# Optimization experiments

Measured on AMD Instinct MI355X. Metric: run time of the kernel, lower is better.

Reference implementation:

```python
import jax, jax.numpy as jnp
import numpy as np
from jax import lax

B, H, W, K, L = 4096, 128, 128, 2, 4
GAMMA = 1e-4  # kernel_gamma
THRESHOLD = 0.0


def setup_inputs() -> dict:
    key = jax.random.key(0)
    ks = jax.random.split(key, 10)
    data = jax.random.normal(ks[0], (B, 1, H, W), jnp.float32)
    conv_w = jax.random.normal(ks[1], (1, 1, K, K), jnp.float32) * 0.5  # OIHW
    conv_b = jax.random.normal(ks[2], (1,), jnp.float32) * 0.1
    # fraud layers: Linear(2,2) weight/bias + affine scale/shift per layer.
    # layers after the first are clamped to [-5,5] at construction time.
    fraud_W = jax.random.normal(ks[3], (L, 2, 2), jnp.float32) * 0.5
    fraud_b = jax.random.normal(ks[4], (L, 2), jnp.float32) * 0.5
    fraud_W = fraud_W.at[1:].set(jnp.clip(fraud_W[1:], -5.0, 5.0))
    fraud_b = fraud_b.at[1:].set(jnp.clip(fraud_b[1:], -5.0, 5.0))
    scale = jax.random.normal(ks[5], (L, 2), jnp.float32)
    shift = jax.random.normal(ks[6], (L, 2), jnp.float32) * 0.1
    final_W = jax.random.normal(ks[7], (1, 2), jnp.float32) * 0.5
    final_b = jax.random.normal(ks[8], (1,), jnp.float32) * 0.1
    return {"data": data, "conv_w": conv_w, "conv_b": conv_b,
            "fraud_W": fraud_W, "fraud_b": fraud_b, "scale": scale,
            "shift": shift, "final_W": final_W, "final_b": final_b}


def reference(data, conv_w, conv_b, fraud_W, fraud_b, scale, shift, final_W, final_b):
    # conv2d(1->1, k=2, valid) + bias, then sigmoid(x - threshold)
    conv = lax.conv_general_dilated(
        data, conv_w, window_strides=(1, 1), padding="VALID",
        dimension_numbers=("NCHW", "OIHW", "NCHW"))
    conv = conv + conv_b[None, :, None, None]
    conv_out = jax.nn.sigmoid(conv - THRESHOLD)
    conv_mean = conv_out.mean(axis=(2, 3))          # [B, 1]
    x = conv_mean.reshape(-1, 2)                    # [B//2, 2] (shape fix)

    def step(carry, p):
        Wl, bl, sl, shl = p
        return jnp.tanh(carry @ Wl.T + bl) * sl + shl, None

    x, _ = lax.scan(step, x, (fraud_W, fraud_b, scale, shift))
    fraud_out = x @ final_W.T + final_b             # [B//2, 1]
    # RBF kernel against zeros over the flattened output -> scalar
    flat = fraud_out.reshape(1, -1)
    k_val = jnp.exp(-GAMMA * jnp.sum(flat * flat, axis=-1, keepdims=True))
    return k_val.squeeze()
```

## Files before the change

kernel.cpp:

```cpp
#include <hip/hip_runtime.h>

#define IMG_H 128
#define IMG_W 128
#define OUT_H 127
#define OUT_W 127

__global__ __launch_bounds__(256) void conv_sig_sum_kernel(
    const float* __restrict__ data,
    const float* __restrict__ conv_w,
    const float* __restrict__ conv_b,
    float* __restrict__ img_sum)
{
    const int b    = blockIdx.x;
    const float* img = data + (size_t)b * (IMG_H * IMG_W);
    const int tid  = threadIdx.x;
    const int wid  = tid >> 6;
    const int lane = tid & 63;

    const float w00 = conv_w[0], w01 = conv_w[1];
    const float w10 = conv_w[2], w11 = conv_w[3];
    const float bias = conv_b[0];

    const int r0 = wid * 32;
    const int r1 = min(r0 + 32, OUT_H);

    float acc = 0.f;

    const float* rt = img + r0 * IMG_W;
    float t0  = rt[lane];
    float t0n = rt[lane + 1];
    float t1  = rt[64 + lane];
    float t1n = (lane < 63) ? rt[65 + lane] : 0.f;

    for (int r = r0; r < r1; ++r) {
        const float* rb = img + (r + 1) * IMG_W;
        float b0  = rb[lane];
        float b0n = rb[lane + 1];
        float b1  = rb[64 + lane];
        float b1n = (lane < 63) ? rb[65 + lane] : 0.f;

        {
            float v = w00 * t0 + w01 * t0n + w10 * b0 + w11 * b0n + bias;
            float e = __expf(-v);
            acc += __builtin_amdgcn_rcpf(1.0f + e);
        }
        if (lane < 63) {
            float v = w00 * t1 + w01 * t1n + w10 * b1 + w11 * b1n + bias;
            float e = __expf(-v);
            acc += __builtin_amdgcn_rcpf(1.0f + e);
        }

        t0 = b0; t0n = b0n; t1 = b1; t1n = b1n;
    }

    #pragma unroll
    for (int off = 32; off > 0; off >>= 1)
        acc += __shfl_down(acc, off, 64);

    __shared__ float wsum[4];
    if (lane == 0) wsum[wid] = acc;
    __syncthreads();
    if (tid == 0)
        img_sum[b] = wsum[0] + wsum[1] + wsum[2] + wsum[3];
}

__global__ __launch_bounds__(256) void fraud_head_kernel(
    const float* __restrict__ img_sum,
    const float* __restrict__ fraud_W,
    const float* __restrict__ fraud_b,
    const float* __restrict__ scale,
    const float* __restrict__ shift,
    const float* __restrict__ final_W,
    const float* __restrict__ final_b,
    float* __restrict__ out)
{
    const int tid = threadIdx.x;
    const float inv_npix = 1.0f / (float)(OUT_H * OUT_W);

    float ssq = 0.f;
    for (int r = tid; r < 2048; r += 256) {
        float x0 = img_sum[2 * r + 0] * inv_npix;
        float x1 = img_sum[2 * r + 1] * inv_npix;
        #pragma unroll
        for (int l = 0; l < 4; ++l) {
            float a00 = fraud_W[l * 4 + 0], a01 = fraud_W[l * 4 + 1];
            float a10 = fraud_W[l * 4 + 2], a11 = fraud_W[l * 4 + 3];
            float y0 = tanhf(x0 * a00 + x1 * a01 + fraud_b[l * 2 + 0])
                           * scale[l * 2 + 0] + shift[l * 2 + 0];
            float y1 = tanhf(x0 * a10 + x1 * a11 + fraud_b[l * 2 + 1])
                           * scale[l * 2 + 1] + shift[l * 2 + 1];
            x0 = y0; x1 = y1;
        }
        float o = x0 * final_W[0] + x1 * final_W[1] + final_b[0];
        ssq += o * o;
    }

    #pragma unroll
    for (int off = 32; off > 0; off >>= 1)
        ssq += __shfl_down(ssq, off, 64);

    __shared__ float wsum[4];
    const int wid = tid >> 6, lane = tid & 63;
    if (lane == 0) wsum[wid] = ssq;
    __syncthreads();
    if (tid == 0) {
        float total = wsum[0] + wsum[1] + wsum[2] + wsum[3];
        out[0] = __expf(-1e-4f * total);
    }
}

extern "C" void kernel_launch(void* const* d_in, const int* in_sizes, int n_in,
                              void* d_out, int out_size, void* d_ws, size_t ws_size,
                              hipStream_t stream) {
    const float* data    = (const float*)d_in[0];
    const float* conv_w  = (const float*)d_in[1];
    const float* conv_b  = (const float*)d_in[2];
    const float* fraud_W = (const float*)d_in[3];
    const float* fraud_b = (const float*)d_in[4];
    const float* scale   = (const float*)d_in[5];
    const float* shift   = (const float*)d_in[6];
    const float* final_W = (const float*)d_in[7];
    const float* final_b = (const float*)d_in[8];
    float* out     = (float*)d_out;
    float* img_sum = (float*)d_ws;

    conv_sig_sum_kernel<<<4096, 256, 0, stream>>>(data, conv_w, conv_b, img_sum);
    fraud_head_kernel<<<1, 256, 0, stream>>>(img_sum, fraud_W, fraud_b,
                                             scale, shift, final_W, final_b, out);
}
```

Baseline: 372.6 us.

## Stage image halves in LDS with float4 loads and split each image across two blocks

```diff
diff --git a/kernel.cpp b/kernel.cpp
--- a/kernel.cpp
+++ b/kernel.cpp
@@ -9,44 +9,63 @@
     const float* __restrict__ data,
     const float* __restrict__ conv_w,
     const float* __restrict__ conv_b,
-    float* __restrict__ img_sum)
+    float* __restrict__ part)
 {
-    const int b    = blockIdx.x;
-    const float* img = data + (size_t)b * (IMG_H * IMG_W);
+    __shared__ float tile[65 * IMG_W];
+
+    const int bid  = blockIdx.x;
+    const int b    = bid >> 1;
+    const int h    = bid & 1;
     const int tid  = threadIdx.x;
     const int wid  = tid >> 6;
     const int lane = tid & 63;
+
+    const int nrows = h ? 64 : 65;
+    const int nout  = h ? 63 : 64;
+
+    const float* src  = data + (size_t)b * (IMG_H * IMG_W) + (h * 64) * IMG_W;
+    const float4* src4 = (const float4*)src;
+    float4* t4 = (float4*)tile;
+
+    float4 v[8];
+    #pragma unroll
+    for (int j = 0; j < 8; ++j) v[j] = src4[tid + j * 256];
+    #pragma unroll
+    for (int j = 0; j < 8; ++j) t4[tid + j * 256] = v[j];
+    if (h == 0 && tid < 32) t4[2048 + tid] = src4[2048 + tid];
+
+    __syncthreads();
 
     const float w00 = conv_w[0], w01 = conv_w[1];
     const float w10 = conv_w[2], w11 = conv_w[3];
     const float bias = conv_b[0];
 
-    const int r0 = wid * 32;
-    const int r1 = min(r0 + 32, OUT_H);
+    const int rs = wid * 16;
+    const int re = min(rs + 16, nout);
 
     float acc = 0.f;
 
-    const float* rt = img + r0 * IMG_W;
-    float t0  = rt[lane];
-    float t0n = rt[lane + 1];
-    float t1  = rt[64 + lane];
-    float t1n = (lane < 63) ? rt[65 + lane] : 0.f;
+    const float* rowt = tile + rs * IMG_W;
+    float t0  = rowt[lane];
+    float t0n = rowt[lane + 1];
+    float t1  = rowt[64 + lane];
+    float t1n = (lane < 63) ? rowt[65 + lane] : 0.f;
 
-    for (int r = r0; r < r1; ++r) {
-        const float* rb = img + (r + 1) * IMG_W;
-        float b0  = rb[lane];
-        float b0n = rb[lane + 1];
-        float b1  = rb[64 + lane];
-        float b1n = (lane < 63) ? rb[65 + lane] : 0.f;
+    for (int r = rs; r < re; ++r) {
+        const float* rowb = tile + (r + 1) * IMG_W;
+        float b0  = rowb[lane];
+        float b0n = rowb[lane + 1];
+        float b1  = rowb[64 + lane];
+        float b1n = (lane < 63) ? rowb[65 + lane] : 0.f;
 
         {
-            float v = w00 * t0 + w01 * t0n + w10 * b0 + w11 * b0n + bias;
-            float e = __expf(-v);
+            float vv = fmaf(w00, t0, fmaf(w01, t0n, fmaf(w10, b0, fmaf(w11, b0n, bias))));
+            float e = __expf(-vv);
             acc += __builtin_amdgcn_rcpf(1.0f + e);
         }
         if (lane < 63) {
-            float v = w00 * t1 + w01 * t1n + w10 * b1 + w11 * b1n + bias;
-            float e = __expf(-v);
+            float vv = fmaf(w00, t1, fmaf(w01, t1n, fmaf(w10, b1, fmaf(w11, b1n, bias))));
+            float e = __expf(-vv);
             acc += __builtin_amdgcn_rcpf(1.0f + e);
         }
 
@@ -61,11 +80,11 @@
     if (lane == 0) wsum[wid] = acc;
     __syncthreads();
     if (tid == 0)
-        img_sum[b] = wsum[0] + wsum[1] + wsum[2] + wsum[3];
+        part[bid] = wsum[0] + wsum[1] + wsum[2] + wsum[3];
 }
 
 __global__ __launch_bounds__(256) void fraud_head_kernel(
-    const float* __restrict__ img_sum,
+    const float* __restrict__ part,
     const float* __restrict__ fraud_W,
     const float* __restrict__ fraud_b,
     const float* __restrict__ scale,
@@ -79,19 +98,19 @@
 
     float ssq = 0.f;
     for (int r = tid; r < 2048; r += 256) {
-        float x0 = img_sum[2 * r + 0] * inv_npix;
-        float x1 = img_sum[2 * r + 1] * inv_npix;
+        float x0 = (part[4 * r + 0] + part[4 * r + 1]) * inv_npix;
+        float x1 = (part[4 * r + 2] + part[4 * r + 3]) * inv_npix;
         #pragma unroll
         for (int l = 0; l < 4; ++l) {
             float a00 = fraud_W[l * 4 + 0], a01 = fraud_W[l * 4 + 1];
             float a10 = fraud_W[l * 4 + 2], a11 = fraud_W[l * 4 + 3];
-            float y0 = tanhf(x0 * a00 + x1 * a01 + fraud_b[l * 2 + 0])
+            float y0 = tanhf(fmaf(x0, a00, fmaf(x1, a01, fraud_b[l * 2 + 0])))
                            * scale[l * 2 + 0] + shift[l * 2 + 0];
-            float y1 = tanhf(x0 * a10 + x1 * a11 + fraud_b[l * 2 + 1])
+            float y1 = tanhf(fmaf(x0, a10, fmaf(x1, a11, fraud_b[l * 2 + 1])))
                            * scale[l * 2 + 1] + shift[l * 2 + 1];
             x0 = y0; x1 = y1;
         }
-        float o = x0 * final_W[0] + x1 * final_W[1] + final_b[0];
+        float o = fmaf(x0, final_W[0], fmaf(x1, final_W[1], final_b[0]));
         ssq += o * o;
     }
 
@@ -121,10 +140,10 @@
     const float* shift   = (const float*)d_in[6];
     const float* final_W = (const float*)d_in[7];
     const float* final_b = (const float*)d_in[8];
-    float* out     = (float*)d_out;
-    float* img_sum = (float*)d_ws;
+    float* out  = (float*)d_out;
+    float* part = (float*)d_ws;
 
-    conv_sig_sum_kernel<<<4096, 256, 0, stream>>>(data, conv_w, conv_b, img_sum);
-    fraud_head_kernel<<<1, 256, 0, stream>>>(img_sum, fraud_W, fraud_b,
+    conv_sig_sum_kernel<<<8192, 256, 0, stream>>>(data, conv_w, conv_b, part);
+    fraud_head_kernel<<<1, 256, 0, stream>>>(part, fraud_W, fraud_b,
                                              scale, shift, final_W, final_b, out);
 }
```

Measured after the change: 375.1 us. No clear change (+0.7%).
